# Kernel optimization log

Hardware: AMD Instinct MI355X
Metric: run time of the kernel (lower is better)

The kernel has to match this reference:

```python
import jax, jax.numpy as jnp
import numpy as np

B, T, H, D = 16, 128, 512, 256
VIN, VOUT = 32000, 32000


def _lstm_cell(xt, h, c, W, U, b):
    # Keras LSTMCell gate order: i, f, g(candidate), o
    z = xt @ W + h @ U + b  # [B, 4H]
    i, f, g, o = jnp.split(z, 4, axis=-1)
    c = jax.nn.sigmoid(f) * c + jax.nn.sigmoid(i) * jnp.tanh(g)
    h = jax.nn.sigmoid(o) * jnp.tanh(c)
    return h, c


def _lstm_seq(x, W, U, b, h0, c0):
    # x: [B,T,Din] -> seq [B,T,H], final (h,c)
    def step(carry, xt):
        h, c = _lstm_cell(xt, carry[0], carry[1], W, U, b)
        return (h, c), h
    (hT, cT), seq = jax.lax.scan(step, (h0, c0), jnp.swapaxes(x, 0, 1))
    return jnp.swapaxes(seq, 0, 1), hT, cT


def setup_inputs() -> dict:
    key = jax.random.key(0)
    ks = jax.random.split(key, 16)
    s = lambda fan: 1.0 / np.sqrt(fan).astype(np.float32)
    f32 = jnp.float32
    return {
        "tokens": jax.random.randint(ks[0], (B, T), 0, VIN + 1),
        "emb": jax.random.normal(ks[1], (VIN + 1, D), f32) * 0.02,
        "W1": jax.random.normal(ks[2], (D, 4 * H), f32) * s(D),
        "U1": jax.random.normal(ks[3], (H, 4 * H), f32) * s(H),
        "b1": jnp.zeros((4 * H,), f32),
        "W2": jax.random.normal(ks[4], (H, 4 * H), f32) * s(H),
        "U2": jax.random.normal(ks[5], (H, 4 * H), f32) * s(H),
        "b2": jnp.zeros((4 * H,), f32),
        "Wd1": jax.random.normal(ks[6], (H, 4 * H), f32) * s(H),
        "Ud1": jax.random.normal(ks[7], (H, 4 * H), f32) * s(H),
        "bd1": jnp.zeros((4 * H,), f32),
        "Wd2": jax.random.normal(ks[8], (H, 4 * H), f32) * s(H),
        "Ud2": jax.random.normal(ks[9], (H, 4 * H), f32) * s(H),
        "bd2": jnp.zeros((4 * H,), f32),
        "Wo": jax.random.normal(ks[10], (2 * H, VOUT + 1), f32) * s(2 * H),
        "bo": jnp.zeros((VOUT + 1,), f32),
    }


def reference(tokens, emb, W1, U1, b1, W2, U2, b2, Wd1, Ud1, bd1, Wd2, Ud2, bd2, Wo, bo):
    x = emb[tokens]  # [B,T,D]
    zeros = jnp.zeros((tokens.shape[0], H), x.dtype)
    seq1, h1, c1 = _lstm_seq(x, W1, U1, b1, zeros, zeros)
    # layer-2 encoder initialized with layer-1 final states (as in source)
    seq2, h2, c2 = _lstm_seq(seq1, W2, U2, b2, h1, c1)

    def dec_step(carry, xt):
        (hA, cA), (hB, cB) = carry
        hA, cA = _lstm_cell(xt, hA, cA, Wd1, Ud1, bd1)
        hB, cB = _lstm_cell(hA, hB, cB, Wd2, Ud2, bd2)
        # global Luong dot attention over full encoder-2 sequence
        score = jax.nn.softmax(jnp.einsum('bsh,bh->bs', seq2, hB), axis=-1)
        ctx = jnp.einsum('bsh,bs->bh', seq2, score)
        out = jnp.concatenate([hB, ctx], axis=-1)  # [B, 2H]
        return ((hA, cA), (hB, cB)), out

    # decoder input is the encoder-2 sequence, time-major
    _, outs = jax.lax.scan(dec_step, ((h1, c1), (h2, c2)), jnp.swapaxes(seq2, 0, 1))
    dec = jnp.swapaxes(outs, 0, 1)  # [B,T,2H]
    logits = dec @ Wo + bo  # [B,T,VOUT+1]
    return jax.nn.softmax(logits, axis=-1)
```

## Files before the change

kernel.cpp:

```cpp
#include <hip/hip_runtime.h>
#include <hip/hip_bf16.h>
#include <math.h>

#define Bq   16
#define Tq   128
#define Hq   512
#define Dq   256
#define G4H  2048
#define MR   2048
#define VO   32001
#define NPAD 32128
#define BH   (Bq * Hq)
#define SENTW 0x7FC0u
#define SENT64 0x7FC07FC07FC07FC0ull
#define SPINCAP (1 << 20)

typedef unsigned int u32;
typedef unsigned long long u64;
typedef __attribute__((ext_vector_type(4))) float f32x4;
typedef __attribute__((ext_vector_type(8))) short bfrag;
typedef __attribute__((ext_vector_type(4))) float facc;

__device__ __forceinline__ float bf2f(short s) {
  union { unsigned u; float f; } v; v.u = ((unsigned)(unsigned short)s) << 16; return v.f;
}
__device__ __forceinline__ short f2bf(float f) {
  union { float f; unsigned u; } v; v.f = f;
  unsigned r = (v.u + 0x7fffu + ((v.u >> 16) & 1u)) >> 16;
  return (short)r;
}
__device__ __forceinline__ float asf(u32 u) {
  union { u32 u; float f; } v; v.u = u; return v.f;
}
__device__ __forceinline__ float sigm(float x) { return 1.0f / (1.0f + expf(-x)); }

__device__ __forceinline__ void ic_store64(u64* p, u64 v) {
  __hip_atomic_store(p, v, __ATOMIC_RELAXED, __HIP_MEMORY_SCOPE_AGENT);
}
__device__ __forceinline__ u64 ic_load64(const u64* p) {
  return __hip_atomic_load(p, __ATOMIC_RELAXED, __HIP_MEMORY_SCOPE_AGENT);
}

__device__ __forceinline__ void* swz(void* plane, int row, int byteoff) {
  return (void*)((char*)plane + row * 1040 + (byteoff ^ ((row & 7) << 4)));
}

__device__ __forceinline__ void stage_h(void* p0, void* p1, const u64 v[8]) {
  #pragma unroll
  for (int it = 0; it < 8; ++it) {
    int i = it * 512 + threadIdx.x;
    int b = i >> 8, bo = (i & 255) * 4;
    *(u32*)swz(p0, b, bo) = (u32)v[it];
    *(u32*)swz(p1, b, bo) = (u32)(v[it] >> 32);
  }
}

__global__ __launch_bounds__(256) void k_fill(u64* __restrict__ p, int n) {
  int i = blockIdx.x * 256 + threadIdx.x;
  if (i < n) p[i] = SENT64;
}

__global__ __launch_bounds__(256) void k_transcvt(const float* __restrict__ in,
                                                  short* __restrict__ out,
                                                  int R, int N, int perm) {
  __shared__ float tile[32][33];
  int nb = blockIdx.x * 32, rb = blockIdx.y * 32;
  int tx = threadIdx.x & 31, ty = threadIdx.x >> 5;
  for (int i = 0; i < 4; ++i) {
    int r = rb + ty + i * 8;
    int n = nb + tx;
    tile[ty + i * 8][tx] = (n < N) ? in[(size_t)r * N + n] : 0.0f;
  }
  __syncthreads();
  for (int i = 0; i < 4; ++i) {
    int n = nb + ty + i * 8;
    int orow = perm ? (((n & 511) << 2) | (n >> 9)) : n;
    out[(size_t)orow * R + rb + tx] = f2bf(tile[tx][ty + i * 8]);
  }
}

__global__ __launch_bounds__(256) void k_gather(const int* __restrict__ tokens,
                                                const float* __restrict__ emb,
                                                short* __restrict__ xbf) {
  int row = blockIdx.x;
  int t = row >> 4, b = row & 15;
  int tok = tokens[b * Tq + t];
  xbf[(size_t)row * Dq + threadIdx.x] = f2bf(emb[(size_t)tok * Dq + threadIdx.x]);
}

__global__ __launch_bounds__(256) void k_gemm(const short* __restrict__ A,
                                              const short* __restrict__ BT,
                                              float* __restrict__ C,
                                              const float* __restrict__ bias,
                                              int M, int Nreal, int K, int ldc,
                                              int permb) {
  __shared__ short lA[128 * 64];
  __shared__ short lB[128 * 64];
  const int tid = threadIdx.x;
  const int wave = tid >> 6, lane = tid & 63;
  const int l15 = lane & 15, l4 = lane >> 4;
  const int m0 = blockIdx.y * 128, n0 = blockIdx.x * 128;
  const int wm = (wave >> 1) * 64, wn = (wave & 1) * 64;
  facc acc[4][4] = {};

  for (int k0 = 0; k0 < K; k0 += 64) {
    __syncthreads();
    for (int i = 0; i < 4; ++i) {
      int c = i * 256 + wave * 64 + lane;
      int r = c >> 3, q = c & 7;
      int qs = q ^ (r & 7);
      const short* ga = A + (size_t)(m0 + r) * K + k0 + qs * 8;
      const short* gb = BT + (size_t)(n0 + r) * K + k0 + qs * 8;
      short* la = lA + (size_t)(i * 256 + wave * 64) * 8;
      short* lb = lB + (size_t)(i * 256 + wave * 64) * 8;
      __builtin_amdgcn_global_load_lds((const __attribute__((address_space(1))) u32*)ga,
                                       (__attribute__((address_space(3))) u32*)la, 16, 0, 0);
      __builtin_amdgcn_global_load_lds((const __attribute__((address_space(1))) u32*)gb,
                                       (__attribute__((address_space(3))) u32*)lb, 16, 0, 0);
    }
    __syncthreads();
    for (int ks = 0; ks < 2; ++ks) {
      bfrag a[4], b[4];
      for (int mi = 0; mi < 4; ++mi) {
        int r = wm + mi * 16 + l15;
        int qs = (ks * 4 + l4) ^ (r & 7);
        a[mi] = *(const bfrag*)&lA[r * 64 + qs * 8];
      }
      for (int ni = 0; ni < 4; ++ni) {
        int r = wn + ni * 16 + l15;
        int qs = (ks * 4 + l4) ^ (r & 7);
        b[ni] = *(const bfrag*)&lB[r * 64 + qs * 8];
      }
      for (int mi = 0; mi < 4; ++mi)
        for (int ni = 0; ni < 4; ++ni)
          acc[mi][ni] = __builtin_amdgcn_mfma_f32_16x16x32_bf16(a[mi], b[ni], acc[mi][ni], 0, 0, 0);
    }
  }
  for (int ni = 0; ni < 4; ++ni) {
    int col = n0 + wn + ni * 16 + l15;
    if (col >= Nreal) continue;
    int bcol = permb ? (((col & 3) << 9) | (col >> 2)) : col;
    float bs = bias ? bias[bcol] : 0.0f;
    for (int mi = 0; mi < 4; ++mi) {
      int rb = m0 + wm + mi * 16 + l4 * 4;
      facc v = acc[mi][ni];
      C[(size_t)(rb + 0) * ldc + col] = v[0] + bs;
      C[(size_t)(rb + 1) * ldc + col] = v[1] + bs;
      C[(size_t)(rb + 2) * ldc + col] = v[2] + bs;
      C[(size_t)(rb + 3) * ldc + col] = v[3] + bs;
    }
  }
}


__global__ __launch_bounds__(512, 1) void k_rec1(const float* __restrict__ XW,
                                                 const short* __restrict__ UT,
                                                 u64* __restrict__ hbuf,
                                                 float* __restrict__ hfin,
                                                 float* __restrict__ cfin) {
  __shared__ short lh[2][16][520];
  __shared__ float zt[8][16][20];
  const int tid = threadIdx.x;
  const int wv = tid >> 6, lane = tid & 63;
  const int l15 = lane & 15, l4 = lane >> 4;
  const int kh = wv >> 2;
  const int gw = blockIdx.x * 4 + (wv & 3);
  const int bb = lane >> 2, jj = lane & 3;
  const int hidx = gw * 4 + jj;

  bfrag ur[8];
  {
    const short* ub = UT + (size_t)(gw * 16 + l15) * Hq + kh * 256 + l4 * 8;
    #pragma unroll
    for (int ks = 0; ks < 8; ++ks) ur[ks] = *(const bfrag*)&ub[ks * 32];
  }
  float c = 0.0f;
  if (wv < 4 && (jj & 1) == 0) {
    ic_store64(&hbuf[(bb * Hq + hidx) >> 1], 0ull);
  }

  for (int s = 0; s < Tq; ++s) {
    f32x4 xg = {};
    if (wv < 4) xg = *(const f32x4*)&XW[(size_t)(s * Bq + bb) * G4H + hidx * 4];
    const u64* hsrc = hbuf + (size_t)s * 4096 + tid;
    u64 v[8];
    for (int spin = 0;; ++spin) {
      #pragma unroll
      for (int it = 0; it < 8; ++it) v[it] = ic_load64(&hsrc[it * 512]);
      u32 bad = 0;
      #pragma unroll
      for (int it = 0; it < 8; ++it) bad |= (((u32)v[it] & 0xFFFFu) == SENTW);
      if (!bad || spin >= SPINCAP) break;
      __builtin_amdgcn_s_sleep(1);
    }
    stage_h(&lh[0][0][0], &lh[1][0][0], v);
    __syncthreads();
    facc a0 = {}, a1 = {};
    #pragma unroll
    for (int ks = 0; ks < 8; ++ks) {
      int bo = kh * 512 + ks * 64 + l4 * 16;
      bfrag ah = *(const bfrag*)swz(&lh[0][0][0], l15, bo);
      bfrag al = *(const bfrag*)swz(&lh[1][0][0], l15, bo);
      a0 = __builtin_amdgcn_mfma_f32_16x16x32_bf16(ah, ur[ks], a0, 0, 0, 0);
      a1 = __builtin_amdgcn_mfma_f32_16x16x32_bf16(al, ur[ks], a1, 0, 0, 0);
    }
    a0 += a1;
    *(f32x4*)&zt[wv][l15][l4 * 4] = a0;
    __syncthreads();
    if (wv < 4) {
      float zi = zt[wv][4 * jj + 0][bb] + zt[wv + 4][4 * jj + 0][bb] + xg[0];
      float zf = zt[wv][4 * jj + 1][bb] + zt[wv + 4][4 * jj + 1][bb] + xg[1];
      float zg = zt[wv][4 * jj + 2][bb] + zt[wv + 4][4 * jj + 2][bb] + xg[2];
      float zo = zt[wv][4 * jj + 3][bb] + zt[wv + 4][4 * jj + 3][bb] + xg[3];
      c = sigm(zf) * c + sigm(zi) * tanhf(zg);
      float hN = sigm(zo) * tanhf(c);
      int hi_ = (int)(unsigned short)f2bf(hN);
      int lo_ = (int)(unsigned short)f2bf(hN - bf2f((short)hi_));
      int hi2 = __shfl_xor(hi_, 1), lo2 = __shfl_xor(lo_, 1);
      if ((jj & 1) == 0) {
        u64 pv = (u64)((u32)hi_ | ((u32)hi2 << 16)) | ((u64)((u32)lo_ | ((u32)lo2 << 16)) << 32);
        ic_store64(&hbuf[(size_t)(s + 1) * 4096 + ((bb * Hq + hidx) >> 1)], pv);
      }
      if (s == Tq - 1) {
        hfin[bb * Hq + hidx] = hN;
        cfin[bb * Hq + hidx] = c;
      }
    }
  }
}

struct CellP {
  const short* ur;
  const short* wr;
  const float* bias;
  const float* hcar;
  const float* ccar;
  u64*  own;
  const u64* inp;
  int   inpPoll;
  short* seq;
  short* dec;
  float* hfin;
  float* cfin;
};
struct Params2 { CellP c[2]; };

__global__ __launch_bounds__(512, 1) void k_cells(Params2 prm) {
  __shared__ short pl[4][16][520];
  __shared__ float zt[8][16][20];
  const int grp = blockIdx.x >> 5, rank = blockIdx.x & 31;
  const CellP P = grp ? prm.c[1] : prm.c[0];
  const int tid = threadIdx.x;
  const int wv = tid >> 6, lane = tid & 63;
  const int l15 = lane & 15, l4 = lane >> 4;
  const int kh = wv >> 2;
  const int gw = rank * 4 + (wv & 3);
  const int bb = lane >> 2, jj = lane & 3;
  const int hidx = gw * 4 + jj;
  const int idx = bb * Hq + hidx;

  bfrag ur[8], wr[8];
  {
    size_t ro = (size_t)(gw * 16 + l15) * Hq + kh * 256 + l4 * 8;
    #pragma unroll
    for (int ks = 0; ks < 8; ++ks) {
      ur[ks] = *(const bfrag*)&P.ur[ro + ks * 32];
      wr[ks] = *(const bfrag*)&P.wr[ro + ks * 32];
    }
  }
  float bi = 0, bf_ = 0, bg_ = 0, bo_ = 0, c = 0.0f;
  if (wv < 4) {
    bi = P.bias[hidx]; bf_ = P.bias[Hq + hidx];
    bg_ = P.bias[2 * Hq + hidx]; bo_ = P.bias[3 * Hq + hidx];
    float hv = P.hcar[idx];
    c = P.ccar[idx];
    int hi_ = (int)(unsigned short)f2bf(hv);
    int lo_ = (int)(unsigned short)f2bf(hv - bf2f((short)hi_));
    int hi2 = __shfl_xor(hi_, 1), lo2 = __shfl_xor(lo_, 1);
    if ((jj & 1) == 0) {
      u64 v = (u64)((u32)hi_ | ((u32)hi2 << 16)) | ((u64)((u32)lo_ | ((u32)lo2 << 16)) << 32);
      ic_store64(&P.own[idx >> 1], v);
    }
  }

  for (int s = 0; s < Tq; ++s) {
    u64 v[8], vx[8];
    const u64* ph = P.own + (size_t)s * 4096 + tid;
    const u64* px = P.inp + (size_t)(s + 1) * 4096 + tid;
    if (P.inpPoll) {
      for (int spin = 0;; ++spin) {
        #pragma unroll
        for (int it = 0; it < 8; ++it) v[it]  = ic_load64(&ph[it * 512]);
        #pragma unroll
        for (int it = 0; it < 8; ++it) vx[it] = ic_load64(&px[it * 512]);
        u32 bad = 0;
        #pragma unroll
        for (int it = 0; it < 8; ++it) {
          bad |= (((u32)v[it]  & 0xFFFFu) == SENTW);
          bad |= (((u32)vx[it] & 0xFFFFu) == SENTW);
        }
        if (!bad || spin >= SPINCAP) break;
        __builtin_amdgcn_s_sleep(1);
      }
    } else {
      #pragma unroll
      for (int it = 0; it < 8; ++it) vx[it] = px[it * 512];
      for (int spin = 0;; ++spin) {
        #pragma unroll
        for (int it = 0; it < 8; ++it) v[it] = ic_load64(&ph[it * 512]);
        u32 bad = 0;
        #pragma unroll
        for (int it = 0; it < 8; ++it) bad |= (((u32)v[it] & 0xFFFFu) == SENTW);
        if (!bad || spin >= SPINCAP) break;
        __builtin_amdgcn_s_sleep(1);
      }
    }
    stage_h(&pl[0][0][0], &pl[1][0][0], v);
    stage_h(&pl[2][0][0], &pl[3][0][0], vx);
    __syncthreads();

    facc a0 = {}, a1 = {}, a2 = {}, a3 = {};
    #pragma unroll
    for (int ks = 0; ks < 8; ++ks) {
      int bo = kh * 512 + ks * 64 + l4 * 16;
      bfrag hh = *(const bfrag*)swz(&pl[0][0][0], l15, bo);
      bfrag hl = *(const bfrag*)swz(&pl[1][0][0], l15, bo);
      bfrag xh = *(const bfrag*)swz(&pl[2][0][0], l15, bo);
      bfrag xl = *(const bfrag*)swz(&pl[3][0][0], l15, bo);
      a0 = __builtin_amdgcn_mfma_f32_16x16x32_bf16(hh, ur[ks], a0, 0, 0, 0);
      a1 = __builtin_amdgcn_mfma_f32_16x16x32_bf16(hl, ur[ks], a1, 0, 0, 0);
      a2 = __builtin_amdgcn_mfma_f32_16x16x32_bf16(xh, wr[ks], a2, 0, 0, 0);
      a3 = __builtin_amdgcn_mfma_f32_16x16x32_bf16(xl, wr[ks], a3, 0, 0, 0);
    }
    a0 += a1; a0 += a2; a0 += a3;
    *(f32x4*)&zt[wv][l15][l4 * 4] = a0;
    __syncthreads();

    if (wv < 4) {
      float zi = zt[wv][4 * jj + 0][bb] + zt[wv + 4][4 * jj + 0][bb] + bi;
      float zf = zt[wv][4 * jj + 1][bb] + zt[wv + 4][4 * jj + 1][bb] + bf_;
      float zg = zt[wv][4 * jj + 2][bb] + zt[wv + 4][4 * jj + 2][bb] + bg_;
      float zo = zt[wv][4 * jj + 3][bb] + zt[wv + 4][4 * jj + 3][bb] + bo_;
      c = sigm(zf) * c + sigm(zi) * tanhf(zg);
      float hN = sigm(zo) * tanhf(c);
      int hi_ = (int)(unsigned short)f2bf(hN);
      int lo_ = (int)(unsigned short)f2bf(hN - bf2f((short)hi_));
      int hi2 = __shfl_xor(hi_, 1), lo2 = __shfl_xor(lo_, 1);
      if ((jj & 1) == 0) {
        u64 pv = (u64)((u32)hi_ | ((u32)hi2 << 16)) | ((u64)((u32)lo_ | ((u32)lo2 << 16)) << 32);
        ic_store64(&P.own[(size_t)(s + 1) * 4096 + (idx >> 1)], pv);
      }
      if (P.seq) P.seq[(size_t)(s * Bq + bb) * Hq + hidx] = (short)hi_;
      if (P.dec) P.dec[((size_t)bb * Tq + s) * (2 * Hq) + hidx] = (short)hi_;
      if (s == Tq - 1 && P.hfin) {
        P.hfin[idx] = hN;
        P.cfin[idx] = c;
      }
    }
  }
}

__global__ __launch_bounds__(256) void k_attn(const short* __restrict__ seq2b,
                                              const short* __restrict__ hqb,
                                              short* __restrict__ decb) {
  int blk = blockIdx.x;
  int b = blk >> 7, t = blk & 127;
  __shared__ u32 q[256];
  __shared__ float part[256];
  __shared__ float p[Tq];
  int tid = threadIdx.x;
  q[tid] = *(const u32*)&hqb[(size_t)(t * Bq + b) * Hq + tid * 2];
  __syncthreads();
  {
    int s = tid >> 1, half = tid & 1;
    const u32* row = (const u32*)&seq2b[(size_t)(s * Bq + b) * Hq + half * 256];
    const u32* qh = q + half * 128;
    float a = 0.0f;
    #pragma unroll 8
    for (int k = 0; k < 128; ++k) {
      u32 r = row[k], qq = qh[k];
      a += asf(r << 16) * asf(qq << 16) + asf(r & 0xFFFF0000u) * asf(qq & 0xFFFF0000u);
    }
    part[tid] = a;
  }
  __syncthreads();
  if (tid < 64) {
    float v0 = part[2 * tid] + part[2 * tid + 1];
    float v1 = part[2 * (tid + 64)] + part[2 * (tid + 64) + 1];
    float mx = fmaxf(v0, v1);
    for (int off = 32; off; off >>= 1) mx = fmaxf(mx, __shfl_xor(mx, off));
    float e0 = __expf(v0 - mx), e1 = __expf(v1 - mx);
    float sm = e0 + e1;
    for (int off = 32; off; off >>= 1) sm += __shfl_xor(sm, off);
    float inv = 1.0f / sm;
    p[tid] = e0 * inv; p[tid + 64] = e1 * inv;
  }
  __syncthreads();
  float c0 = 0.0f, c1 = 0.0f;
  for (int s = 0; s < Tq; ++s) {
    float ps = p[s];
    u32 r = *(const u32*)&seq2b[(size_t)(s * Bq + b) * Hq + tid * 2];
    c0 += ps * asf(r << 16);
    c1 += ps * asf(r & 0xFFFF0000u);
  }
  u32 o = ((u32)(unsigned short)f2bf(c0)) | (((u32)(unsigned short)f2bf(c1)) << 16);
  *(u32*)&decb[(size_t)(b * Tq + t) * (2 * Hq) + Hq + tid * 2] = o;
}

__global__ __launch_bounds__(256) void k_softmax(float* __restrict__ L) {
  int row = blockIdx.x;
  float* p = L + (size_t)row * VO;
  int tid = threadIdx.x;
  float m = -3.0e38f, s = 0.0f;
  for (int i = tid; i < VO; i += 256) {
    float v = p[i];
    float mn = fmaxf(m, v);
    s = s * __expf(m - mn) + __expf(v - mn);
    m = mn;
  }
  __shared__ float sm[256], ss[256];
  sm[tid] = m; ss[tid] = s;
  __syncthreads();
  for (int off = 128; off; off >>= 1) {
    if (tid < off) {
      float m2 = sm[tid + off], s2 = ss[tid + off];
      float mn = fmaxf(sm[tid], m2);
      ss[tid] = ss[tid] * __expf(sm[tid] - mn) + s2 * __expf(m2 - mn);
      sm[tid] = mn;
    }
    __syncthreads();
  }
  float M = sm[0], IS = 1.0f / ss[0];
  for (int i = tid; i < VO; i += 256) {
    p[i] = __expf(p[i] - M) * IS;
  }
}

extern "C" void kernel_launch(void* const* d_in, const int* in_sizes, int n_in,
                              void* d_out, int out_size, void* d_ws, size_t ws_size,
                              hipStream_t stream) {
  const int*   tokens = (const int*)d_in[0];
  const float* emb    = (const float*)d_in[1];
  const float* W1     = (const float*)d_in[2];
  const float* U1     = (const float*)d_in[3];
  const float* b1     = (const float*)d_in[4];
  const float* W2     = (const float*)d_in[5];
  const float* U2     = (const float*)d_in[6];
  const float* b2     = (const float*)d_in[7];
  const float* Wd1    = (const float*)d_in[8];
  const float* Ud1    = (const float*)d_in[9];
  const float* bd1    = (const float*)d_in[10];
  const float* Wd2    = (const float*)d_in[11];
  const float* Ud2    = (const float*)d_in[12];
  const float* bd2    = (const float*)d_in[13];
  const float* Wo     = (const float*)d_in[14];
  const float* bo     = (const float*)d_in[15];
  float* out = (float*)d_out;

  size_t off = 0;
  char* base = (char*)d_ws;
  auto alloc = [&](size_t bytes) -> void* {
    void* p = base + off;
    off += (bytes + 255) & ~(size_t)255;
    return p;
  };
  short* x_bf    = (short*)alloc((size_t)MR * Dq * 2);
  short* W1T     = (short*)alloc((size_t)G4H * Dq * 2);
  short* WoT     = (short*)alloc((size_t)NPAD * (2 * Hq) * 2);
  short* U1T     = (short*)alloc((size_t)G4H * Hq * 2);
  short* U2T     = (short*)alloc((size_t)G4H * Hq * 2);
  short* W2T     = (short*)alloc((size_t)G4H * Hq * 2);
  short* Ud1T    = (short*)alloc((size_t)G4H * Hq * 2);
  short* Wd1T    = (short*)alloc((size_t)G4H * Hq * 2);
  short* Ud2T    = (short*)alloc((size_t)G4H * Hq * 2);
  short* Wd2T    = (short*)alloc((size_t)G4H * Hq * 2);
  float* XW      = (float*)alloc((size_t)MR * G4H * 4);
  short* seq2_bf = (short*)alloc((size_t)MR * Hq * 2);
  short* hBseqbf = (short*)alloc((size_t)MR * Hq * 2);
  short* dec_bf  = (short*)alloc((size_t)MR * 2 * Hq * 2);
  u64*   hflow   = (u64*)alloc((size_t)516 * 4096 * 8);
  float* h1f     = (float*)alloc(BH * 4);
  float* c1f     = (float*)alloc(BH * 4);
  float* h2f     = (float*)alloc(BH * 4);
  float* c2f     = (float*)alloc(BH * 4);
  u64* h1buf = hflow;
  u64* h2buf = hflow + (size_t)129 * 4096;
  u64* hAbuf = hflow + (size_t)258 * 4096;
  u64* hBbuf = hflow + (size_t)387 * 4096;
  (void)ws_size; (void)in_sizes; (void)n_in; (void)out_size;

  {
    int n64 = 516 * 4096;
    k_fill<<<(n64 + 255) / 256, 256, 0, stream>>>(hflow, n64);
  }

  k_transcvt<<<dim3(G4H / 32, Dq / 32), 256, 0, stream>>>(W1, W1T, Dq, G4H, 1);
  k_transcvt<<<dim3(G4H / 32, Hq / 32), 256, 0, stream>>>(U1, U1T, Hq, G4H, 1);
  k_transcvt<<<dim3(G4H / 32, Hq / 32), 256, 0, stream>>>(U2, U2T, Hq, G4H, 1);
  k_transcvt<<<dim3(G4H / 32, Hq / 32), 256, 0, stream>>>(W2, W2T, Hq, G4H, 1);
  k_transcvt<<<dim3(G4H / 32, Hq / 32), 256, 0, stream>>>(Ud1, Ud1T, Hq, G4H, 1);
  k_transcvt<<<dim3(G4H / 32, Hq / 32), 256, 0, stream>>>(Wd1, Wd1T, Hq, G4H, 1);
  k_transcvt<<<dim3(G4H / 32, Hq / 32), 256, 0, stream>>>(Ud2, Ud2T, Hq, G4H, 1);
  k_transcvt<<<dim3(G4H / 32, Hq / 32), 256, 0, stream>>>(Wd2, Wd2T, Hq, G4H, 1);
  k_transcvt<<<dim3(NPAD / 32, (2 * Hq) / 32), 256, 0, stream>>>(Wo, WoT, 2 * Hq, VO, 0);

  k_gather<<<MR, 256, 0, stream>>>(tokens, emb, x_bf);

  k_gemm<<<dim3(G4H / 128, MR / 128), 256, 0, stream>>>(x_bf, W1T, XW, b1, MR, G4H, Dq, G4H, 1);
  k_rec1<<<32, 512, 0, stream>>>(XW, U1T, h1buf, h1f, c1f);

  {
    Params2 p;
    p.c[0] = { U2T, W2T, b2,  h1f, c1f, h2buf, h1buf, 0, seq2_bf, nullptr, h2f, c2f };
    p.c[1] = { Ud1T, Wd1T, bd1, h1f, c1f, hAbuf, h2buf, 1, nullptr, nullptr, nullptr, nullptr };
    k_cells<<<64, 512, 0, stream>>>(p);
  }

  {
    Params2 p;
    p.c[0] = { Ud2T, Wd2T, bd2, h2f, c2f, hBbuf, hAbuf, 0, hBseqbf, dec_bf, nullptr, nullptr };
    p.c[1] = p.c[0];
    k_cells<<<32, 512, 0, stream>>>(p);
  }

  k_attn<<<MR, 256, 0, stream>>>(seq2_bf, hBseqbf, dec_bf);
  k_gemm<<<dim3(NPAD / 128, MR / 128), 256, 0, stream>>>(dec_bf, WoT, out, bo, MR, VO, 2 * Hq, VO, 0);
  k_softmax<<<MR, 256, 0, stream>>>(out);
}
```

Baseline: 2.395 ms.

## Replace per-thread sentinel spin polling with per-block step counter flags

Adds per-block progress counters, each padded to its own stride. A block publishes its counter after waiting for its stores and a block barrier. When the sentinel check fails, consumers no longer have all 512 threads spin-load the full h buffer. Instead 32 threads poll the producer flags, and a block-wide OR decides whether to retry. This cuts polling traffic on the h exchange buffers across the recurrent kernels, but adds an extra barrier and memory fence on every timestep.

```diff
diff --git a/kernel.cpp b/kernel.cpp
--- a/kernel.cpp
+++ b/kernel.cpp
@@ -14,6 +14,7 @@
 #define SENTW 0x7FC0u
 #define SENT64 0x7FC07FC07FC07FC0ull
 #define SPINCAP (1 << 20)
+#define FSTRIDE 32
 
 typedef unsigned int u32;
 typedef unsigned long long u64;
@@ -38,6 +39,12 @@
   __hip_atomic_store(p, v, __ATOMIC_RELAXED, __HIP_MEMORY_SCOPE_AGENT);
 }
 __device__ __forceinline__ u64 ic_load64(const u64* p) {
+  return __hip_atomic_load(p, __ATOMIC_RELAXED, __HIP_MEMORY_SCOPE_AGENT);
+}
+__device__ __forceinline__ void ic_store32(u32* p, u32 v) {
+  __hip_atomic_store(p, v, __ATOMIC_RELAXED, __HIP_MEMORY_SCOPE_AGENT);
+}
+__device__ __forceinline__ u32 ic_load32(const u32* p) {
   return __hip_atomic_load(p, __ATOMIC_RELAXED, __HIP_MEMORY_SCOPE_AGENT);
 }
 
@@ -55,9 +62,40 @@
   }
 }
 
+__device__ __forceinline__ void waitf(const u32* f, u32 need) {
+  if (threadIdx.x < 32) {
+    u32 v; int spin = 0;
+    do {
+      v = ic_load32(&f[threadIdx.x * FSTRIDE]);
+      if (v < need) __builtin_amdgcn_s_sleep(2);
+    } while (v < need && ++spin < SPINCAP);
+  }
+  __syncthreads();
+}
+__device__ __forceinline__ void waitf2(const u32* fa, u32 na, const u32* fb, u32 nb) {
+  if (threadIdx.x < 32) {
+    u32 v; int spin = 0;
+    do {
+      v = ic_load32(&fa[threadIdx.x * FSTRIDE]);
+      if (v < na) __builtin_amdgcn_s_sleep(2);
+    } while (v < na && ++spin < SPINCAP);
+  } else if (threadIdx.x >= 64 && threadIdx.x < 96) {
+    u32 v; int spin = 0;
+    do {
+      v = ic_load32(&fb[(threadIdx.x - 64) * FSTRIDE]);
+      if (v < nb) __builtin_amdgcn_s_sleep(2);
+    } while (v < nb && ++spin < SPINCAP);
+  }
+  __syncthreads();
+}
+
 __global__ __launch_bounds__(256) void k_fill(u64* __restrict__ p, int n) {
   int i = blockIdx.x * 256 + threadIdx.x;
   if (i < n) p[i] = SENT64;
+}
+__global__ __launch_bounds__(256) void k_fill0(u32* __restrict__ p, int n) {
+  int i = blockIdx.x * 256 + threadIdx.x;
+  if (i < n) p[i] = 0u;
 }
 
 __global__ __launch_bounds__(256) void k_transcvt(const float* __restrict__ in,
@@ -156,15 +194,17 @@
 __global__ __launch_bounds__(512, 1) void k_rec1(const float* __restrict__ XW,
                                                  const short* __restrict__ UT,
                                                  u64* __restrict__ hbuf,
+                                                 u32* __restrict__ fown,
                                                  float* __restrict__ hfin,
                                                  float* __restrict__ cfin) {
   __shared__ short lh[2][16][520];
   __shared__ float zt[8][16][20];
+  const int rank = blockIdx.x;
   const int tid = threadIdx.x;
   const int wv = tid >> 6, lane = tid & 63;
   const int l15 = lane & 15, l4 = lane >> 4;
   const int kh = wv >> 2;
-  const int gw = blockIdx.x * 4 + (wv & 3);
+  const int gw = rank * 4 + (wv & 3);
   const int bb = lane >> 2, jj = lane & 3;
   const int hidx = gw * 4 + jj;
 
@@ -175,23 +215,25 @@
     for (int ks = 0; ks < 8; ++ks) ur[ks] = *(const bfrag*)&ub[ks * 32];
   }
   float c = 0.0f;
-  if (wv < 4 && (jj & 1) == 0) {
+  if (wv < 4 && (jj & 1) == 0)
     ic_store64(&hbuf[(bb * Hq + hidx) >> 1], 0ull);
-  }
+  asm volatile("s_waitcnt vmcnt(0)" ::: "memory");
+  __syncthreads();
+  if (tid == 0) ic_store32(&fown[rank * FSTRIDE], 1u);
 
   for (int s = 0; s < Tq; ++s) {
     f32x4 xg = {};
     if (wv < 4) xg = *(const f32x4*)&XW[(size_t)(s * Bq + bb) * G4H + hidx * 4];
-    const u64* hsrc = hbuf + (size_t)s * 4096 + tid;
+    const u64* ph = hbuf + (size_t)s * 4096 + tid;
     u64 v[8];
-    for (int spin = 0;; ++spin) {
+    for (int tries = 0;; ++tries) {
       #pragma unroll
-      for (int it = 0; it < 8; ++it) v[it] = ic_load64(&hsrc[it * 512]);
+      for (int it = 0; it < 8; ++it) v[it] = ic_load64(&ph[it * 512]);
       u32 bad = 0;
       #pragma unroll
       for (int it = 0; it < 8; ++it) bad |= (((u32)v[it] & 0xFFFFu) == SENTW);
-      if (!bad || spin >= SPINCAP) break;
-      __builtin_amdgcn_s_sleep(1);
+      if (!__syncthreads_or((int)bad) || tries >= 8) break;
+      waitf(fown, (u32)(s + 1));
     }
     stage_h(&lh[0][0][0], &lh[1][0][0], v);
     __syncthreads();
@@ -221,11 +263,11 @@
         u64 pv = (u64)((u32)hi_ | ((u32)hi2 << 16)) | ((u64)((u32)lo_ | ((u32)lo2 << 16)) << 32);
         ic_store64(&hbuf[(size_t)(s + 1) * 4096 + ((bb * Hq + hidx) >> 1)], pv);
       }
-      if (s == Tq - 1) {
-        hfin[bb * Hq + hidx] = hN;
-        cfin[bb * Hq + hidx] = c;
-      }
-    }
+      if (s == Tq - 1) { hfin[bb * Hq + hidx] = hN; cfin[bb * Hq + hidx] = c; }
+    }
+    asm volatile("s_waitcnt vmcnt(0)" ::: "memory");
+    __syncthreads();
+    if (tid == 0) ic_store32(&fown[rank * FSTRIDE], (u32)(s + 2));
   }
 }
 
@@ -237,7 +279,8 @@
   const float* ccar;
   u64*  own;
   const u64* inp;
-  int   inpPoll;
+  u32*  fOwn;
+  const u32* fInp;
   short* seq;
   short* dec;
   float* hfin;
@@ -282,13 +325,16 @@
       ic_store64(&P.own[idx >> 1], v);
     }
   }
+  asm volatile("s_waitcnt vmcnt(0)" ::: "memory");
+  __syncthreads();
+  if (tid == 0) ic_store32(&P.fOwn[rank * FSTRIDE], 1u);
 
   for (int s = 0; s < Tq; ++s) {
     u64 v[8], vx[8];
     const u64* ph = P.own + (size_t)s * 4096 + tid;
     const u64* px = P.inp + (size_t)(s + 1) * 4096 + tid;
-    if (P.inpPoll) {
-      for (int spin = 0;; ++spin) {
+    if (P.fInp) {
+      for (int tries = 0;; ++tries) {
         #pragma unroll
         for (int it = 0; it < 8; ++it) v[it]  = ic_load64(&ph[it * 512]);
         #pragma unroll
@@ -299,20 +345,20 @@
           bad |= (((u32)v[it]  & 0xFFFFu) == SENTW);
           bad |= (((u32)vx[it] & 0xFFFFu) == SENTW);
         }
-        if (!bad || spin >= SPINCAP) break;
-        __builtin_amdgcn_s_sleep(1);
+        if (!__syncthreads_or((int)bad) || tries >= 8) break;
+        waitf2(P.fOwn, (u32)(s + 1), P.fInp, (u32)(s + 2));
       }
     } else {
       #pragma unroll
       for (int it = 0; it < 8; ++it) vx[it] = px[it * 512];
-      for (int spin = 0;; ++spin) {
+      for (int tries = 0;; ++tries) {
         #pragma unroll
         for (int it = 0; it < 8; ++it) v[it] = ic_load64(&ph[it * 512]);
         u32 bad = 0;
         #pragma unroll
         for (int it = 0; it < 8; ++it) bad |= (((u32)v[it] & 0xFFFFu) == SENTW);
-        if (!bad || spin >= SPINCAP) break;
-        __builtin_amdgcn_s_sleep(1);
+        if (!__syncthreads_or((int)bad) || tries >= 8) break;
+        waitf(P.fOwn, (u32)(s + 1));
       }
     }
     stage_h(&pl[0][0][0], &pl[1][0][0], v);
@@ -352,11 +398,11 @@
       }
       if (P.seq) P.seq[(size_t)(s * Bq + bb) * Hq + hidx] = (short)hi_;
       if (P.dec) P.dec[((size_t)bb * Tq + s) * (2 * Hq) + hidx] = (short)hi_;
-      if (s == Tq - 1 && P.hfin) {
-        P.hfin[idx] = hN;
-        P.cfin[idx] = c;
-      }
-    }
+      if (s == Tq - 1 && P.hfin) { P.hfin[idx] = hN; P.cfin[idx] = c; }
+    }
+    asm volatile("s_waitcnt vmcnt(0)" ::: "memory");
+    __syncthreads();
+    if (tid == 0) ic_store32(&P.fOwn[rank * FSTRIDE], (u32)(s + 2));
   }
 }
 
@@ -479,6 +525,7 @@
   short* hBseqbf = (short*)alloc((size_t)MR * Hq * 2);
   short* dec_bf  = (short*)alloc((size_t)MR * 2 * Hq * 2);
   u64*   hflow   = (u64*)alloc((size_t)516 * 4096 * 8);
+  u32*   flags   = (u32*)alloc(4 * 32 * FSTRIDE * 4);
   float* h1f     = (float*)alloc(BH * 4);
   float* c1f     = (float*)alloc(BH * 4);
   float* h2f     = (float*)alloc(BH * 4);
@@ -487,11 +534,16 @@
   u64* h2buf = hflow + (size_t)129 * 4096;
   u64* hAbuf = hflow + (size_t)258 * 4096;
   u64* hBbuf = hflow + (size_t)387 * 4096;
+  u32* f1 = flags;
+  u32* f2 = flags + 32 * FSTRIDE;
+  u32* fA = flags + 64 * FSTRIDE;
+  u32* fB = flags + 96 * FSTRIDE;
   (void)ws_size; (void)in_sizes; (void)n_in; (void)out_size;
 
   {
     int n64 = 516 * 4096;
     k_fill<<<(n64 + 255) / 256, 256, 0, stream>>>(hflow, n64);
+    k_fill0<<<(4 * 32 * FSTRIDE + 255) / 256, 256, 0, stream>>>(flags, 4 * 32 * FSTRIDE);
   }
 
   k_transcvt<<<dim3(G4H / 32, Dq / 32), 256, 0, stream>>>(W1, W1T, Dq, G4H, 1);
@@ -507,18 +559,21 @@
   k_gather<<<MR, 256, 0, stream>>>(tokens, emb, x_bf);
 
   k_gemm<<<dim3(G4H / 128, MR / 128), 256, 0, stream>>>(x_bf, W1T, XW, b1, MR, G4H, Dq, G4H, 1);
-  k_rec1<<<32, 512, 0, stream>>>(XW, U1T, h1buf, h1f, c1f);
+  k_rec1<<<32, 512, 0, stream>>>(XW, U1T, h1buf, f1, h1f, c1f);
 
   {
     Params2 p;
-    p.c[0] = { U2T, W2T, b2,  h1f, c1f, h2buf, h1buf, 0, seq2_bf, nullptr, h2f, c2f };
-    p.c[1] = { Ud1T, Wd1T, bd1, h1f, c1f, hAbuf, h2buf, 1, nullptr, nullptr, nullptr, nullptr };
+    p.c[0] = { U2T, W2T, b2,  h1f, c1f, h2buf, h1buf, f2, nullptr,
+               seq2_bf, nullptr, h2f, c2f };
+    p.c[1] = { Ud1T, Wd1T, bd1, h1f, c1f, hAbuf, h2buf, fA, f2,
+               nullptr, nullptr, nullptr, nullptr };
     k_cells<<<64, 512, 0, stream>>>(p);
   }
 
   {
     Params2 p;
-    p.c[0] = { Ud2T, Wd2T, bd2, h2f, c2f, hBbuf, hAbuf, 0, hBseqbf, dec_bf, nullptr, nullptr };
+    p.c[0] = { Ud2T, Wd2T, bd2, h2f, c2f, hBbuf, hAbuf, fB, nullptr,
+               hBseqbf, dec_bf, nullptr, nullptr };
     p.c[1] = p.c[0];
     k_cells<<<32, 512, 0, stream>>>(p);
   }
```

New measurement: 2.575 ms. +7.5%, slower.
